# Performance work log

Measured on AMD Instinct MI355X. Metric: run time of the kernel, lower is better.

Reference implementation:

```python
import jax, jax.numpy as jnp
import numpy as np


def _dynamics(x, ts, W1, b1, tW, W2, b2, W3, b3):
    # 2-hidden-layer tanh MLP with additive time conditioning; works for [B,D] or [D].
    h = jnp.tanh(x @ W1 + b1 + ts * tW)
    h = jnp.tanh(h @ W2 + b2)
    return h @ W3 + b3


def setup_inputs() -> dict:
    key = jax.random.key(0)
    B, D, H = 1024, 256, 1024
    ks = jax.random.split(key, 8)
    scaled = lambda k, shape, fan: jax.random.normal(k, shape, jnp.float32) / np.float32(np.sqrt(fan))
    return {
        "x": jax.random.normal(ks[0], (B, D), jnp.float32),
        "t": jax.random.uniform(ks[1], (1,), jnp.float32),
        "ldj": jnp.zeros((B,), jnp.float32),
        "reg_term": jnp.zeros((B,), jnp.float32),
        "W1": scaled(ks[2], (D, H), D),
        "b1": jnp.zeros((H,), jnp.float32),
        "tW": scaled(ks[3], (H,), 1),
        "W2": scaled(ks[4], (H, H), H),
        "b2": jnp.zeros((H,), jnp.float32),
        "W3": scaled(ks[5], (H, D), H),
        "b3": jnp.zeros((D,), jnp.float32),
    }


def reference(x, t, ldj, reg_term, W1, b1, tW, W2, b2, W3, b3):
    ts = t[0]
    # dx = dynamics(x, t)
    dx = _dynamics(x, ts, W1, b1, tW, W2, b2, W3, b3)
    # exact trace of per-sample Jacobian d dynamics / dx  (trace_method='exact')
    f_single = lambda xi: _dynamics(xi, ts, W1, b1, tW, W2, b2, W3, b3)  # [D] -> [D]
    jac = jax.vmap(jax.jacfwd(f_single))(x)          # [B, D, D]
    ldj_out = jnp.trace(jac, axis1=1, axis2=2)       # [B]
    reg_out = jnp.zeros_like(ldj_out)                 # ode_regularization == 0
    return dx, ldj_out, reg_out
```

## Files before the change

kernel.cpp:

```cpp
#include <hip/hip_runtime.h>
#include <math.h>

#define Bsz 1024
#define Dsz 256
#define Hsz 1024

typedef unsigned short u16;
typedef __bf16 bf16x8 __attribute__((ext_vector_type(8)));
typedef float  f32x4  __attribute__((ext_vector_type(4)));

__device__ __forceinline__ float bf2f(u16 u) {
  unsigned v = ((unsigned)u) << 16;
  return __builtin_bit_cast(float, v);
}
__device__ __forceinline__ u16 f2bf(float f) {
  unsigned u = __builtin_bit_cast(unsigned, f);
  u += 0x7FFFu + ((u >> 16) & 1u);
  return (u16)(u >> 16);
}

__device__ __forceinline__ void cast_chunk(const float* __restrict__ in,
                                           u16* __restrict__ out, int b, int t) {
  const int i = b * 256 + t;
  const float4 v = reinterpret_cast<const float4*>(in)[i];
  ushort4 o;
  o.x = f2bf(v.x); o.y = f2bf(v.y); o.z = f2bf(v.z); o.w = f2bf(v.w);
  *reinterpret_cast<ushort4*>(&out[(size_t)i * 4]) = o;
}

__device__ __forceinline__ void tr_tile(float (*tl)[65], const float* __restrict__ in,
                                        u16* __restrict__ out, int R, int C,
                                        int c0, int r0, int t) {
#pragma unroll
  for (int p = 0; p < 4; ++p) {
    const int r = p * 16 + (t >> 4);
    const int c = (t & 15) * 4;
    const float4 v = *reinterpret_cast<const float4*>(&in[(size_t)(r0 + r) * C + c0 + c]);
    tl[r][c] = v.x; tl[r][c + 1] = v.y; tl[r][c + 2] = v.z; tl[r][c + 3] = v.w;
  }
  __syncthreads();
#pragma unroll
  for (int p = 0; p < 4; ++p) {
    const int a = p * 16 + (t >> 4);
    const int b4 = (t & 15) * 4;
    ushort4 o;
    o.x = f2bf(tl[b4 + 0][a]); o.y = f2bf(tl[b4 + 1][a]);
    o.z = f2bf(tl[b4 + 2][a]); o.w = f2bf(tl[b4 + 3][a]);
    *reinterpret_cast<ushort4*>(&out[(size_t)(c0 + a) * R + r0 + b4]) = o;
  }
}

__global__ __launch_bounds__(256) void prep(const float* __restrict__ x,
                                            const float* __restrict__ W1,
                                            const float* __restrict__ W2,
                                            const float* __restrict__ W3,
                                            u16* __restrict__ xb,
                                            u16* __restrict__ W3b,
                                            u16* __restrict__ W1bT,
                                            u16* __restrict__ W2bT,
                                            u16* __restrict__ W3bT,
                                            float* __restrict__ ldj) {
  __shared__ float tl[64][65];
  const int b = blockIdx.x, t = threadIdx.x;
  if (b == 0) {
    for (int i = t; i < 2048; i += 256) ldj[i] = 0.0f;
  }
  if (b < 256) {
    cast_chunk(x, xb, b, t);
  } else if (b < 512) {
    cast_chunk(W3, W3b, b - 256, t);
  } else if (b < 576) {
    const int tb = b - 512;
    tr_tile(tl, W1, W1bT, Dsz, Hsz, (tb & 15) * 64, (tb >> 4) * 64, t);
  } else if (b < 832) {
    const int tb = b - 576;
    tr_tile(tl, W2, W2bT, Hsz, Hsz, (tb & 15) * 64, (tb >> 4) * 64, t);
  } else {
    const int tb = b - 832;
    tr_tile(tl, W3, W3bT, Hsz, Dsz, (tb & 3) * 64, (tb >> 2) * 64, t);
  }
}

enum { EPI_H1 = 0, EPI_AMAT = 1, EPI_H2 = 2, EPI_DX = 3, EPI_TRACE = 4 };
constexpr int LS = 72;

template <int EPI, bool SQA>
__device__ __forceinline__ void gemm_body(
    int row0, int col0,
    u16* __restrict__ As, u16* __restrict__ Bs, float (*sred)[33],
    const u16* __restrict__ A, const u16* __restrict__ Bt,
    int K, int ldo,
    float* __restrict__ fout, u16* __restrict__ bout,
    const u16* __restrict__ aux,
    const float* __restrict__ v1, const float* __restrict__ v2,
    const float* __restrict__ tptr) {
  const int t = threadIdx.x;
  const int lane = t & 63, wid = t >> 6;

  const int sm = t >> 2, sq = t & 3;
  const size_t a_base = (size_t)(row0 + sm) * K + sq * 8;
  const size_t b_base = (size_t)(col0 + sm) * K + sq * 8;

  uint4 ar[2], br[2];
  auto load_regs = [&](int k0) {
    ar[0] = *reinterpret_cast<const uint4*>(&A[a_base + k0]);
    ar[1] = *reinterpret_cast<const uint4*>(&A[a_base + k0 + 32]);
    br[0] = *reinterpret_cast<const uint4*>(&Bt[b_base + k0]);
    br[1] = *reinterpret_cast<const uint4*>(&Bt[b_base + k0 + 32]);
  };
  auto sq_tr = [&](uint4 v) -> uint4 {
    u16* p = reinterpret_cast<u16*>(&v);
    uint4 o; u16* po = reinterpret_cast<u16*>(&o);
#pragma unroll
    for (int i = 0; i < 8; ++i) { const float h = bf2f(p[i]); po[i] = f2bf(1.0f - h * h); }
    return o;
  };
  auto store_lds = [&]() {
    const int ab = sm * LS + sq * 8;
#pragma unroll
    for (int c = 0; c < 2; ++c) {
      const uint4 av = SQA ? sq_tr(ar[c]) : ar[c];
      *reinterpret_cast<uint4*>(&As[ab + c * 32]) = av;
      *reinterpret_cast<uint4*>(&Bs[ab + c * 32]) = br[c];
    }
  };

  f32x4 acc[2][2] = {};
  const int mo = (wid >> 1) * 32, no = (wid & 1) * 32;
  const int fr = lane & 15, fg = lane >> 4;

  const int NK = K >> 6;
  load_regs(0);
  for (int it = 0; it < NK; ++it) {
    __syncthreads();
    store_lds();
    if (it + 1 < NK) load_regs((it + 1) << 6);
    __syncthreads();
#pragma unroll
    for (int ks = 0; ks < 64; ks += 32) {
      union { uint4 u; bf16x8 b; } cv;
      cv.u = *reinterpret_cast<const uint4*>(&As[(mo + fr) * LS + ks + fg * 8]);
      const bf16x8 a0 = cv.b;
      cv.u = *reinterpret_cast<const uint4*>(&As[(mo + 16 + fr) * LS + ks + fg * 8]);
      const bf16x8 a1 = cv.b;
      cv.u = *reinterpret_cast<const uint4*>(&Bs[(no + fr) * LS + ks + fg * 8]);
      const bf16x8 b0 = cv.b;
      cv.u = *reinterpret_cast<const uint4*>(&Bs[(no + 16 + fr) * LS + ks + fg * 8]);
      const bf16x8 b1 = cv.b;
      acc[0][0] = __builtin_amdgcn_mfma_f32_16x16x32_bf16(a0, b0, acc[0][0], 0, 0, 0);
      acc[0][1] = __builtin_amdgcn_mfma_f32_16x16x32_bf16(a0, b1, acc[0][1], 0, 0, 0);
      acc[1][0] = __builtin_amdgcn_mfma_f32_16x16x32_bf16(a1, b0, acc[1][0], 0, 0, 0);
      acc[1][1] = __builtin_amdgcn_mfma_f32_16x16x32_bf16(a1, b1, acc[1][1], 0, 0, 0);
    }
  }

  const int cr = mo + fg * 4;
  const int cc = no + fr;

  if (EPI == EPI_H1) {
    const float ts = tptr[0];
#pragma unroll
    for (int ni = 0; ni < 2; ++ni) {
      const int col = col0 + cc + ni * 16;
      const float add = v1[col] + ts * v2[col];
#pragma unroll
      for (int mi = 0; mi < 2; ++mi)
#pragma unroll
        for (int r = 0; r < 4; ++r) {
          const int row = row0 + cr + mi * 16 + r;
          bout[(size_t)row * Hsz + col] = f2bf(tanhf(acc[mi][ni][r] + add));
        }
    }
  } else if (EPI == EPI_AMAT) {
#pragma unroll
    for (int mi = 0; mi < 2; ++mi)
#pragma unroll
      for (int ni = 0; ni < 2; ++ni)
#pragma unroll
        for (int r = 0; r < 4; ++r) {
          const int row = row0 + cr + mi * 16 + r;
          const int col = col0 + cc + ni * 16;
          const float w2 = bf2f(aux[(size_t)row * Hsz + col]);
          bout[(size_t)row * Hsz + col] = f2bf(w2 * acc[mi][ni][r]);
        }
  } else if (EPI == EPI_H2) {
#pragma unroll
    for (int ni = 0; ni < 2; ++ni) {
      const int col = col0 + cc + ni * 16;
      const float add = v1[col];
#pragma unroll
      for (int mi = 0; mi < 2; ++mi)
#pragma unroll
        for (int r = 0; r < 4; ++r) {
          const int row = row0 + cr + mi * 16 + r;
          bout[(size_t)row * Hsz + col] = f2bf(tanhf(acc[mi][ni][r] + add));
        }
    }
  } else if (EPI == EPI_DX) {
#pragma unroll
    for (int ni = 0; ni < 2; ++ni) {
      const int col = col0 + cc + ni * 16;
      const float add = v1[col];
#pragma unroll
      for (int mi = 0; mi < 2; ++mi)
#pragma unroll
        for (int r = 0; r < 4; ++r) {
          const int row = row0 + cr + mi * 16 + r;
          fout[(size_t)row * ldo + col] = acc[mi][ni][r] + add;
        }
    }
  } else {
#pragma unroll
    for (int mi = 0; mi < 2; ++mi)
#pragma unroll
      for (int r = 0; r < 4; ++r) {
        const int row = row0 + cr + mi * 16 + r;
        float s = 0.f;
#pragma unroll
        for (int ni = 0; ni < 2; ++ni) {
          const int col = col0 + cc + ni * 16;
          const float h2 = bf2f(aux[(size_t)row * Hsz + col]);
          s += acc[mi][ni][r] * (1.0f - h2 * h2);
        }
        sred[cr + mi * 16 + r][(wid & 1) * 16 + fr] = s;
      }
    __syncthreads();
    if (t < 64) {
      float s = 0.f;
#pragma unroll
      for (int u = 0; u < 32; ++u) s += sred[t][u];
      atomicAdd(&fout[row0 + t], s);
    }
  }
}

__global__ __launch_bounds__(256) void phaseB(const u16* __restrict__ xb,
                                              const u16* __restrict__ W1bT,
                                              const u16* __restrict__ W3b,
                                              const u16* __restrict__ W2bT,
                                              u16* __restrict__ H1b,
                                              u16* __restrict__ AmatT,
                                              const float* __restrict__ b1,
                                              const float* __restrict__ tW,
                                              const float* __restrict__ t) {
  __shared__ u16 As[64 * LS];
  __shared__ u16 Bs[64 * LS];
  const int b = blockIdx.x;
  if (b < 256) {
    gemm_body<EPI_H1, false>((b >> 4) * 64, (b & 15) * 64, As, Bs, nullptr,
                             xb, W1bT, Dsz, Hsz, nullptr, H1b, nullptr, b1, tW, t);
  } else {
    const int c = b - 256;
    gemm_body<EPI_AMAT, false>((c >> 4) * 64, (c & 15) * 64, As, Bs, nullptr,
                               W3b, W1bT, Dsz, Hsz, nullptr, AmatT, W2bT,
                               nullptr, nullptr, nullptr);
  }
}

__global__ __launch_bounds__(256) void phaseC(const u16* __restrict__ H1b,
                                              const u16* __restrict__ W2bT,
                                              u16* __restrict__ H2b,
                                              const float* __restrict__ b2) {
  __shared__ u16 As[64 * LS];
  __shared__ u16 Bs[64 * LS];
  const int b = blockIdx.x;
  gemm_body<EPI_H2, false>((b >> 4) * 64, (b & 15) * 64, As, Bs, nullptr,
                           H1b, W2bT, Hsz, Hsz, nullptr, H2b, nullptr, b2,
                           nullptr, nullptr);
}

__global__ __launch_bounds__(256) void phaseD(const u16* __restrict__ H1b,
                                              const u16* __restrict__ AmatT,
                                              const u16* __restrict__ H2b,
                                              const u16* __restrict__ W3bT,
                                              float* __restrict__ ldj,
                                              float* __restrict__ dx,
                                              const float* __restrict__ b3) {
  __shared__ u16 As[64 * LS];
  __shared__ u16 Bs[64 * LS];
  __shared__ float sred[64][33];
  const int b = blockIdx.x;
  if (b < 256) {
    gemm_body<EPI_TRACE, true>((b >> 4) * 64, (b & 15) * 64, As, Bs, sred,
                               H1b, AmatT, Hsz, 0, ldj, nullptr, H2b,
                               nullptr, nullptr, nullptr);
  } else {
    const int c = b - 256;
    gemm_body<EPI_DX, false>((c >> 2) * 64, (c & 3) * 64, As, Bs, nullptr,
                             H2b, W3bT, Hsz, Dsz, dx, nullptr, nullptr, b3,
                             nullptr, nullptr);
  }
}

extern "C" void kernel_launch(void* const* d_in, const int* in_sizes, int n_in,
                              void* d_out, int out_size, void* d_ws, size_t ws_size,
                              hipStream_t stream) {
  const float* x  = (const float*)d_in[0];
  const float* t  = (const float*)d_in[1];
  const float* W1 = (const float*)d_in[4];
  const float* b1 = (const float*)d_in[5];
  const float* tW = (const float*)d_in[6];
  const float* W2 = (const float*)d_in[7];
  const float* b2 = (const float*)d_in[8];
  const float* W3 = (const float*)d_in[9];
  const float* b3 = (const float*)d_in[10];

  float* out = (float*)d_out;
  float* dx  = out;
  float* ldj = out + (size_t)Bsz * Dsz;

  u16* w = (u16*)d_ws;
  u16* xb    = w;
  u16* W1bT  = xb    + 262144;
  u16* W3b   = W1bT  + 262144;
  u16* W3bT  = W3b   + 262144;
  u16* W2bT  = W3bT  + 262144;
  u16* AmatT = W2bT  + 1048576;
  u16* H1b   = AmatT + 1048576;
  u16* H2b   = H1b   + 1048576;

  const dim3 blk(256);
  prep  <<<dim3(896), blk, 0, stream>>>(x, W1, W2, W3, xb, W3b, W1bT, W2bT, W3bT, ldj);
  phaseB<<<dim3(512), blk, 0, stream>>>(xb, W1bT, W3b, W2bT, H1b, AmatT, b1, tW, t);
  phaseC<<<dim3(256), blk, 0, stream>>>(H1b, W2bT, H2b, b2);
  phaseD<<<dim3(320), blk, 0, stream>>>(H1b, AmatT, H2b, W3bT, ldj, dx, b3);
}
```

Baseline: 133.9 us.

## Fuse paired GEMMs sharing operands and recompute H2 inside trace kernel

Merges the H1 and Amat GEMMs into one kernel that shares the W1 tile loads. It also merges the H2 GEMM with the trace GEMM: H1 tiles are loaded once, tanh is recomputed in registers, and H2 is written while the trace is accumulated without being re-read. The dx GEMM moves to a separate 64-block kernel, and block indices are swizzled for L2 locality. This cuts redundant global loads and one round trip for H2. In exchange there are fewer blocks per launch, more LDS per block, and a small dx launch that underfills the GPU.

```diff
diff --git a/kernel.cpp b/kernel.cpp
--- a/kernel.cpp
+++ b/kernel.cpp
@@ -18,6 +18,15 @@
   u += 0x7FFFu + ((u >> 16) & 1u);
   return (u16)(u >> 16);
 }
+
+constexpr int LS = 72;
+
+__device__ __forceinline__ bf16x8 frag(const u16* __restrict__ s, int row, int off) {
+  union { uint4 u; bf16x8 b; } cv;
+  cv.u = *reinterpret_cast<const uint4*>(&s[row * LS + off]);
+  return cv.b;
+}
+#define MFMA __builtin_amdgcn_mfma_f32_16x16x32_bf16
 
 __device__ __forceinline__ void cast_chunk(const float* __restrict__ in,
                                            u16* __restrict__ out, int b, int t) {
@@ -81,32 +90,119 @@
   }
 }
 
-enum { EPI_H1 = 0, EPI_AMAT = 1, EPI_H2 = 2, EPI_DX = 3, EPI_TRACE = 4 };
-constexpr int LS = 72;
-
-template <int EPI, bool SQA>
-__device__ __forceinline__ void gemm_body(
-    int row0, int col0,
-    u16* __restrict__ As, u16* __restrict__ Bs, float (*sred)[33],
-    const u16* __restrict__ A, const u16* __restrict__ Bt,
-    int K, int ldo,
-    float* __restrict__ fout, u16* __restrict__ bout,
-    const u16* __restrict__ aux,
-    const float* __restrict__ v1, const float* __restrict__ v2,
-    const float* __restrict__ tptr) {
+__global__ __launch_bounds__(256) void phaseBB(const u16* __restrict__ xb,
+                                               const u16* __restrict__ W3b,
+                                               const u16* __restrict__ W1bT,
+                                               const u16* __restrict__ W2bT,
+                                               u16* __restrict__ H1b,
+                                               u16* __restrict__ AmatT,
+                                               const float* __restrict__ b1,
+                                               const float* __restrict__ tW,
+                                               const float* __restrict__ tptr) {
+  __shared__ u16 A1s[64 * LS];
+  __shared__ u16 A2s[64 * LS];
+  __shared__ u16 Bs[64 * LS];
   const int t = threadIdx.x;
   const int lane = t & 63, wid = t >> 6;
+  const int bz = ((blockIdx.x & 7) << 5) + (blockIdx.x >> 3);
+  const int row0 = (bz >> 4) * 64, col0 = (bz & 15) * 64;
 
   const int sm = t >> 2, sq = t & 3;
-  const size_t a_base = (size_t)(row0 + sm) * K + sq * 8;
-  const size_t b_base = (size_t)(col0 + sm) * K + sq * 8;
-
-  uint4 ar[2], br[2];
+  const size_t ab = (size_t)(row0 + sm) * Dsz + sq * 8;
+  const size_t bb = (size_t)(col0 + sm) * Dsz + sq * 8;
+
+  uint4 a1r[2], a2r[2], br[2];
   auto load_regs = [&](int k0) {
-    ar[0] = *reinterpret_cast<const uint4*>(&A[a_base + k0]);
-    ar[1] = *reinterpret_cast<const uint4*>(&A[a_base + k0 + 32]);
-    br[0] = *reinterpret_cast<const uint4*>(&Bt[b_base + k0]);
-    br[1] = *reinterpret_cast<const uint4*>(&Bt[b_base + k0 + 32]);
+    a1r[0] = *reinterpret_cast<const uint4*>(&xb[ab + k0]);
+    a1r[1] = *reinterpret_cast<const uint4*>(&xb[ab + k0 + 32]);
+    a2r[0] = *reinterpret_cast<const uint4*>(&W3b[ab + k0]);
+    a2r[1] = *reinterpret_cast<const uint4*>(&W3b[ab + k0 + 32]);
+    br[0]  = *reinterpret_cast<const uint4*>(&W1bT[bb + k0]);
+    br[1]  = *reinterpret_cast<const uint4*>(&W1bT[bb + k0 + 32]);
+  };
+  auto store_lds = [&]() {
+    const int o = sm * LS + sq * 8;
+#pragma unroll
+    for (int c = 0; c < 2; ++c) {
+      *reinterpret_cast<uint4*>(&A1s[o + c * 32]) = a1r[c];
+      *reinterpret_cast<uint4*>(&A2s[o + c * 32]) = a2r[c];
+      *reinterpret_cast<uint4*>(&Bs[o + c * 32])  = br[c];
+    }
+  };
+
+  f32x4 acc1[2][2] = {}, acc2[2][2] = {};
+  const int mo = (wid >> 1) * 32, no = (wid & 1) * 32;
+  const int fr = lane & 15, fg = lane >> 4;
+
+  load_regs(0);
+  for (int it = 0; it < Dsz / 64; ++it) {
+    __syncthreads();
+    store_lds();
+    if (it + 1 < Dsz / 64) load_regs((it + 1) << 6);
+    __syncthreads();
+#pragma unroll
+    for (int ks = 0; ks < 64; ks += 32) {
+      const int off = ks + fg * 8;
+      const bf16x8 a10 = frag(A1s, mo + fr, off), a11 = frag(A1s, mo + 16 + fr, off);
+      const bf16x8 a20 = frag(A2s, mo + fr, off), a21 = frag(A2s, mo + 16 + fr, off);
+      const bf16x8 b0  = frag(Bs,  no + fr, off), b1v = frag(Bs,  no + 16 + fr, off);
+      acc1[0][0] = MFMA(a10, b0,  acc1[0][0], 0, 0, 0);
+      acc1[0][1] = MFMA(a10, b1v, acc1[0][1], 0, 0, 0);
+      acc1[1][0] = MFMA(a11, b0,  acc1[1][0], 0, 0, 0);
+      acc1[1][1] = MFMA(a11, b1v, acc1[1][1], 0, 0, 0);
+      acc2[0][0] = MFMA(a20, b0,  acc2[0][0], 0, 0, 0);
+      acc2[0][1] = MFMA(a20, b1v, acc2[0][1], 0, 0, 0);
+      acc2[1][0] = MFMA(a21, b0,  acc2[1][0], 0, 0, 0);
+      acc2[1][1] = MFMA(a21, b1v, acc2[1][1], 0, 0, 0);
+    }
+  }
+
+  const int cr = mo + fg * 4, cc = no + fr;
+  const float ts = tptr[0];
+#pragma unroll
+  for (int ni = 0; ni < 2; ++ni) {
+    const int col = col0 + cc + ni * 16;
+    const float add = b1[col] + ts * tW[col];
+#pragma unroll
+    for (int mi = 0; mi < 2; ++mi)
+#pragma unroll
+      for (int r = 0; r < 4; ++r) {
+        const int row = row0 + cr + mi * 16 + r;
+        H1b[(size_t)row * Hsz + col] = f2bf(tanhf(acc1[mi][ni][r] + add));
+        const float w2 = bf2f(W2bT[(size_t)row * Hsz + col]);
+        AmatT[(size_t)row * Hsz + col] = f2bf(w2 * acc2[mi][ni][r]);
+      }
+  }
+}
+
+__global__ __launch_bounds__(256) void phaseCD(const u16* __restrict__ H1b,
+                                               const u16* __restrict__ W2bT,
+                                               const u16* __restrict__ AmatT,
+                                               u16* __restrict__ H2b,
+                                               float* __restrict__ ldj,
+                                               const float* __restrict__ b2) {
+  __shared__ u16 Ars[64 * LS];
+  __shared__ u16 Ads[64 * LS];
+  __shared__ u16 B1s[64 * LS];
+  __shared__ u16 B2s[64 * LS];
+  __shared__ float sred[64][33];
+  const int t = threadIdx.x;
+  const int lane = t & 63, wid = t >> 6;
+  const int bz = ((blockIdx.x & 7) << 5) + (blockIdx.x >> 3);
+  const int row0 = (bz >> 4) * 64, col0 = (bz & 15) * 64;
+
+  const int sm = t >> 2, sq = t & 3;
+  const size_t ab = (size_t)(row0 + sm) * Hsz + sq * 8;
+  const size_t bb = (size_t)(col0 + sm) * Hsz + sq * 8;
+
+  uint4 ar[2], b1r[2], b2r[2];
+  auto load_regs = [&](int k0) {
+    ar[0]  = *reinterpret_cast<const uint4*>(&H1b[ab + k0]);
+    ar[1]  = *reinterpret_cast<const uint4*>(&H1b[ab + k0 + 32]);
+    b1r[0] = *reinterpret_cast<const uint4*>(&W2bT[bb + k0]);
+    b1r[1] = *reinterpret_cast<const uint4*>(&W2bT[bb + k0 + 32]);
+    b2r[0] = *reinterpret_cast<const uint4*>(&AmatT[bb + k0]);
+    b2r[1] = *reinterpret_cast<const uint4*>(&AmatT[bb + k0 + 32]);
   };
   auto sq_tr = [&](uint4 v) -> uint4 {
     u16* p = reinterpret_cast<u16*>(&v);
@@ -116,179 +212,134 @@
     return o;
   };
   auto store_lds = [&]() {
-    const int ab = sm * LS + sq * 8;
+    const int o = sm * LS + sq * 8;
 #pragma unroll
     for (int c = 0; c < 2; ++c) {
-      const uint4 av = SQA ? sq_tr(ar[c]) : ar[c];
-      *reinterpret_cast<uint4*>(&As[ab + c * 32]) = av;
-      *reinterpret_cast<uint4*>(&Bs[ab + c * 32]) = br[c];
-    }
-  };
-
-  f32x4 acc[2][2] = {};
+      *reinterpret_cast<uint4*>(&Ars[o + c * 32]) = ar[c];
+      *reinterpret_cast<uint4*>(&Ads[o + c * 32]) = sq_tr(ar[c]);
+      *reinterpret_cast<uint4*>(&B1s[o + c * 32]) = b1r[c];
+      *reinterpret_cast<uint4*>(&B2s[o + c * 32]) = b2r[c];
+    }
+  };
+
+  f32x4 acc1[2][2] = {}, acc2[2][2] = {};
   const int mo = (wid >> 1) * 32, no = (wid & 1) * 32;
   const int fr = lane & 15, fg = lane >> 4;
 
-  const int NK = K >> 6;
   load_regs(0);
-  for (int it = 0; it < NK; ++it) {
+  for (int it = 0; it < Hsz / 64; ++it) {
     __syncthreads();
     store_lds();
-    if (it + 1 < NK) load_regs((it + 1) << 6);
+    if (it + 1 < Hsz / 64) load_regs((it + 1) << 6);
     __syncthreads();
 #pragma unroll
     for (int ks = 0; ks < 64; ks += 32) {
-      union { uint4 u; bf16x8 b; } cv;
-      cv.u = *reinterpret_cast<const uint4*>(&As[(mo + fr) * LS + ks + fg * 8]);
-      const bf16x8 a0 = cv.b;
-      cv.u = *reinterpret_cast<const uint4*>(&As[(mo + 16 + fr) * LS + ks + fg * 8]);
-      const bf16x8 a1 = cv.b;
-      cv.u = *reinterpret_cast<const uint4*>(&Bs[(no + fr) * LS + ks + fg * 8]);
-      const bf16x8 b0 = cv.b;
-      cv.u = *reinterpret_cast<const uint4*>(&Bs[(no + 16 + fr) * LS + ks + fg * 8]);
-      const bf16x8 b1 = cv.b;
-      acc[0][0] = __builtin_amdgcn_mfma_f32_16x16x32_bf16(a0, b0, acc[0][0], 0, 0, 0);
-      acc[0][1] = __builtin_amdgcn_mfma_f32_16x16x32_bf16(a0, b1, acc[0][1], 0, 0, 0);
-      acc[1][0] = __builtin_amdgcn_mfma_f32_16x16x32_bf16(a1, b0, acc[1][0], 0, 0, 0);
-      acc[1][1] = __builtin_amdgcn_mfma_f32_16x16x32_bf16(a1, b1, acc[1][1], 0, 0, 0);
-    }
-  }
-
-  const int cr = mo + fg * 4;
-  const int cc = no + fr;
-
-  if (EPI == EPI_H1) {
-    const float ts = tptr[0];
-#pragma unroll
-    for (int ni = 0; ni < 2; ++ni) {
-      const int col = col0 + cc + ni * 16;
-      const float add = v1[col] + ts * v2[col];
-#pragma unroll
-      for (int mi = 0; mi < 2; ++mi)
-#pragma unroll
-        for (int r = 0; r < 4; ++r) {
-          const int row = row0 + cr + mi * 16 + r;
-          bout[(size_t)row * Hsz + col] = f2bf(tanhf(acc[mi][ni][r] + add));
-        }
-    }
-  } else if (EPI == EPI_AMAT) {
-#pragma unroll
-    for (int mi = 0; mi < 2; ++mi)
-#pragma unroll
-      for (int ni = 0; ni < 2; ++ni)
-#pragma unroll
-        for (int r = 0; r < 4; ++r) {
-          const int row = row0 + cr + mi * 16 + r;
-          const int col = col0 + cc + ni * 16;
-          const float w2 = bf2f(aux[(size_t)row * Hsz + col]);
-          bout[(size_t)row * Hsz + col] = f2bf(w2 * acc[mi][ni][r]);
-        }
-  } else if (EPI == EPI_H2) {
-#pragma unroll
-    for (int ni = 0; ni < 2; ++ni) {
-      const int col = col0 + cc + ni * 16;
-      const float add = v1[col];
-#pragma unroll
-      for (int mi = 0; mi < 2; ++mi)
-#pragma unroll
-        for (int r = 0; r < 4; ++r) {
-          const int row = row0 + cr + mi * 16 + r;
-          bout[(size_t)row * Hsz + col] = f2bf(tanhf(acc[mi][ni][r] + add));
-        }
-    }
-  } else if (EPI == EPI_DX) {
-#pragma unroll
-    for (int ni = 0; ni < 2; ++ni) {
-      const int col = col0 + cc + ni * 16;
-      const float add = v1[col];
-#pragma unroll
-      for (int mi = 0; mi < 2; ++mi)
-#pragma unroll
-        for (int r = 0; r < 4; ++r) {
-          const int row = row0 + cr + mi * 16 + r;
-          fout[(size_t)row * ldo + col] = acc[mi][ni][r] + add;
-        }
-    }
-  } else {
-#pragma unroll
-    for (int mi = 0; mi < 2; ++mi)
-#pragma unroll
-      for (int r = 0; r < 4; ++r) {
+      const int off = ks + fg * 8;
+      const bf16x8 x0 = frag(Ars, mo + fr, off), x1 = frag(Ars, mo + 16 + fr, off);
+      const bf16x8 d0 = frag(Ads, mo + fr, off), d1 = frag(Ads, mo + 16 + fr, off);
+      const bf16x8 w0 = frag(B1s, no + fr, off), w1 = frag(B1s, no + 16 + fr, off);
+      const bf16x8 m0 = frag(B2s, no + fr, off), m1 = frag(B2s, no + 16 + fr, off);
+      acc1[0][0] = MFMA(x0, w0, acc1[0][0], 0, 0, 0);
+      acc1[0][1] = MFMA(x0, w1, acc1[0][1], 0, 0, 0);
+      acc1[1][0] = MFMA(x1, w0, acc1[1][0], 0, 0, 0);
+      acc1[1][1] = MFMA(x1, w1, acc1[1][1], 0, 0, 0);
+      acc2[0][0] = MFMA(d0, m0, acc2[0][0], 0, 0, 0);
+      acc2[0][1] = MFMA(d0, m1, acc2[0][1], 0, 0, 0);
+      acc2[1][0] = MFMA(d1, m0, acc2[1][0], 0, 0, 0);
+      acc2[1][1] = MFMA(d1, m1, acc2[1][1], 0, 0, 0);
+    }
+  }
+
+  const int cr = mo + fg * 4, cc = no + fr;
+#pragma unroll
+  for (int mi = 0; mi < 2; ++mi)
+#pragma unroll
+    for (int r = 0; r < 4; ++r) {
+      float s = 0.f;
+#pragma unroll
+      for (int ni = 0; ni < 2; ++ni) {
+        const int col = col0 + cc + ni * 16;
         const int row = row0 + cr + mi * 16 + r;
-        float s = 0.f;
-#pragma unroll
-        for (int ni = 0; ni < 2; ++ni) {
-          const int col = col0 + cc + ni * 16;
-          const float h2 = bf2f(aux[(size_t)row * Hsz + col]);
-          s += acc[mi][ni][r] * (1.0f - h2 * h2);
-        }
-        sred[cr + mi * 16 + r][(wid & 1) * 16 + fr] = s;
+        const float h = tanhf(acc1[mi][ni][r] + b2[col]);
+        H2b[(size_t)row * Hsz + col] = f2bf(h);
+        s += acc2[mi][ni][r] * (1.0f - h * h);
       }
-    __syncthreads();
-    if (t < 64) {
-      float s = 0.f;
-#pragma unroll
-      for (int u = 0; u < 32; ++u) s += sred[t][u];
-      atomicAdd(&fout[row0 + t], s);
-    }
-  }
-}
-
-__global__ __launch_bounds__(256) void phaseB(const u16* __restrict__ xb,
-                                              const u16* __restrict__ W1bT,
-                                              const u16* __restrict__ W3b,
-                                              const u16* __restrict__ W2bT,
-                                              u16* __restrict__ H1b,
-                                              u16* __restrict__ AmatT,
-                                              const float* __restrict__ b1,
-                                              const float* __restrict__ tW,
-                                              const float* __restrict__ t) {
-  __shared__ u16 As[64 * LS];
-  __shared__ u16 Bs[64 * LS];
-  const int b = blockIdx.x;
-  if (b < 256) {
-    gemm_body<EPI_H1, false>((b >> 4) * 64, (b & 15) * 64, As, Bs, nullptr,
-                             xb, W1bT, Dsz, Hsz, nullptr, H1b, nullptr, b1, tW, t);
-  } else {
-    const int c = b - 256;
-    gemm_body<EPI_AMAT, false>((c >> 4) * 64, (c & 15) * 64, As, Bs, nullptr,
-                               W3b, W1bT, Dsz, Hsz, nullptr, AmatT, W2bT,
-                               nullptr, nullptr, nullptr);
-  }
-}
-
-__global__ __launch_bounds__(256) void phaseC(const u16* __restrict__ H1b,
-                                              const u16* __restrict__ W2bT,
-                                              u16* __restrict__ H2b,
-                                              const float* __restrict__ b2) {
-  __shared__ u16 As[64 * LS];
-  __shared__ u16 Bs[64 * LS];
-  const int b = blockIdx.x;
-  gemm_body<EPI_H2, false>((b >> 4) * 64, (b & 15) * 64, As, Bs, nullptr,
-                           H1b, W2bT, Hsz, Hsz, nullptr, H2b, nullptr, b2,
-                           nullptr, nullptr);
-}
-
-__global__ __launch_bounds__(256) void phaseD(const u16* __restrict__ H1b,
-                                              const u16* __restrict__ AmatT,
-                                              const u16* __restrict__ H2b,
+      sred[cr + mi * 16 + r][(wid & 1) * 16 + fr] = s;
+    }
+  __syncthreads();
+  if (t < 64) {
+    float s = 0.f;
+#pragma unroll
+    for (int u = 0; u < 32; ++u) s += sred[t][u];
+    atomicAdd(&ldj[row0 + t], s);
+  }
+}
+
+__global__ __launch_bounds__(256) void phaseE(const u16* __restrict__ H2b,
                                               const u16* __restrict__ W3bT,
-                                              float* __restrict__ ldj,
                                               float* __restrict__ dx,
                                               const float* __restrict__ b3) {
   __shared__ u16 As[64 * LS];
   __shared__ u16 Bs[64 * LS];
-  __shared__ float sred[64][33];
-  const int b = blockIdx.x;
-  if (b < 256) {
-    gemm_body<EPI_TRACE, true>((b >> 4) * 64, (b & 15) * 64, As, Bs, sred,
-                               H1b, AmatT, Hsz, 0, ldj, nullptr, H2b,
-                               nullptr, nullptr, nullptr);
-  } else {
-    const int c = b - 256;
-    gemm_body<EPI_DX, false>((c >> 2) * 64, (c & 3) * 64, As, Bs, nullptr,
-                             H2b, W3bT, Hsz, Dsz, dx, nullptr, nullptr, b3,
-                             nullptr, nullptr);
+  const int t = threadIdx.x;
+  const int lane = t & 63, wid = t >> 6;
+  const int bz = ((blockIdx.x & 7) << 3) + (blockIdx.x >> 3);
+  const int row0 = (bz >> 2) * 64, col0 = (bz & 3) * 64;
+
+  const int sm = t >> 2, sq = t & 3;
+  const size_t ab = (size_t)(row0 + sm) * Hsz + sq * 8;
+  const size_t bb = (size_t)(col0 + sm) * Hsz + sq * 8;
+
+  uint4 ar[2], br[2];
+  auto load_regs = [&](int k0) {
+    ar[0] = *reinterpret_cast<const uint4*>(&H2b[ab + k0]);
+    ar[1] = *reinterpret_cast<const uint4*>(&H2b[ab + k0 + 32]);
+    br[0] = *reinterpret_cast<const uint4*>(&W3bT[bb + k0]);
+    br[1] = *reinterpret_cast<const uint4*>(&W3bT[bb + k0 + 32]);
+  };
+  auto store_lds = [&]() {
+    const int o = sm * LS + sq * 8;
+#pragma unroll
+    for (int c = 0; c < 2; ++c) {
+      *reinterpret_cast<uint4*>(&As[o + c * 32]) = ar[c];
+      *reinterpret_cast<uint4*>(&Bs[o + c * 32]) = br[c];
+    }
+  };
+
+  f32x4 acc[2][2] = {};
+  const int mo = (wid >> 1) * 32, no = (wid & 1) * 32;
+  const int fr = lane & 15, fg = lane >> 4;
+
+  load_regs(0);
+  for (int it = 0; it < Hsz / 64; ++it) {
+    __syncthreads();
+    store_lds();
+    if (it + 1 < Hsz / 64) load_regs((it + 1) << 6);
+    __syncthreads();
+#pragma unroll
+    for (int ks = 0; ks < 64; ks += 32) {
+      const int off = ks + fg * 8;
+      const bf16x8 a0 = frag(As, mo + fr, off), a1 = frag(As, mo + 16 + fr, off);
+      const bf16x8 b0 = frag(Bs, no + fr, off), b1v = frag(Bs, no + 16 + fr, off);
+      acc[0][0] = MFMA(a0, b0,  acc[0][0], 0, 0, 0);
+      acc[0][1] = MFMA(a0, b1v, acc[0][1], 0, 0, 0);
+      acc[1][0] = MFMA(a1, b0,  acc[1][0], 0, 0, 0);
+      acc[1][1] = MFMA(a1, b1v, acc[1][1], 0, 0, 0);
+    }
+  }
+
+  const int cr = mo + fg * 4, cc = no + fr;
+#pragma unroll
+  for (int ni = 0; ni < 2; ++ni) {
+    const int col = col0 + cc + ni * 16;
+    const float add = b3[col];
+#pragma unroll
+    for (int mi = 0; mi < 2; ++mi)
+#pragma unroll
+      for (int r = 0; r < 4; ++r) {
+        const int row = row0 + cr + mi * 16 + r;
+        dx[(size_t)row * Dsz + col] = acc[mi][ni][r] + add;
+      }
   }
 }
 
@@ -320,8 +371,8 @@
   u16* H2b   = H1b   + 1048576;
 
   const dim3 blk(256);
-  prep  <<<dim3(896), blk, 0, stream>>>(x, W1, W2, W3, xb, W3b, W1bT, W2bT, W3bT, ldj);
-  phaseB<<<dim3(512), blk, 0, stream>>>(xb, W1bT, W3b, W2bT, H1b, AmatT, b1, tW, t);
-  phaseC<<<dim3(256), blk, 0, stream>>>(H1b, W2bT, H2b, b2);
-  phaseD<<<dim3(320), blk, 0, stream>>>(H1b, AmatT, H2b, W3bT, ldj, dx, b3);
-}
+  prep   <<<dim3(896), blk, 0, stream>>>(x, W1, W2, W3, xb, W3b, W1bT, W2bT, W3bT, ldj);
+  phaseBB<<<dim3(256), blk, 0, stream>>>(xb, W3b, W1bT, W2bT, H1b, AmatT, b1, tW, t);
+  phaseCD<<<dim3(256), blk, 0, stream>>>(H1b, W2bT, AmatT, H2b, ldj, b2);
+  phaseE <<<dim3(64),  blk, 0, stream>>>(H2b, W3bT, dx, b3);
+}
```

Result: slower. 159.5 us (+19.1%).

## Move trace GEMM into phase C and reduce trace in a light phase D

Applied to the files above, without the earlier changes.

The large trace GEMM (H1' times AmatT) moves from phaseD into phaseC, where it runs alongside the H2 GEMM because it does not depend on H2. It writes an fp32 intermediate U, and a small reduction in phaseD multiplies U by (1-h2^2) and sums each row into ldj. This removes the serial tail where phaseD ran 256 heavy GEMM blocks after phaseC, and drops the per-block atomics. In exchange it adds a 4 MB fp32 write and read of U. Note the SQA path still applies 1-h^2 to H1, and ldj is now written directly rather than accumulated.

```diff
diff --git a/kernel.cpp b/kernel.cpp
--- a/kernel.cpp
+++ b/kernel.cpp
@@ -18,6 +18,15 @@
   u += 0x7FFFu + ((u >> 16) & 1u);
   return (u16)(u >> 16);
 }
+
+constexpr int LS = 72;
+
+__device__ __forceinline__ bf16x8 frag(const u16* __restrict__ s, int row, int off) {
+  union { uint4 u; bf16x8 b; } cv;
+  cv.u = *reinterpret_cast<const uint4*>(&s[row * LS + off]);
+  return cv.b;
+}
+#define MFMA __builtin_amdgcn_mfma_f32_16x16x32_bf16
 
 __device__ __forceinline__ void cast_chunk(const float* __restrict__ in,
                                            u16* __restrict__ out, int b, int t) {
@@ -81,13 +90,12 @@
   }
 }
 
-enum { EPI_H1 = 0, EPI_AMAT = 1, EPI_H2 = 2, EPI_DX = 3, EPI_TRACE = 4 };
-constexpr int LS = 72;
+enum { EPI_H1 = 0, EPI_AMAT = 1, EPI_H2 = 2, EPI_DX = 3, EPI_U = 4 };
 
 template <int EPI, bool SQA>
 __device__ __forceinline__ void gemm_body(
     int row0, int col0,
-    u16* __restrict__ As, u16* __restrict__ Bs, float (*sred)[33],
+    u16* __restrict__ As, u16* __restrict__ Bs,
     const u16* __restrict__ A, const u16* __restrict__ Bt,
     int K, int ldo,
     float* __restrict__ fout, u16* __restrict__ bout,
@@ -116,12 +124,11 @@
     return o;
   };
   auto store_lds = [&]() {
-    const int ab = sm * LS + sq * 8;
+    const int o = sm * LS + sq * 8;
 #pragma unroll
     for (int c = 0; c < 2; ++c) {
-      const uint4 av = SQA ? sq_tr(ar[c]) : ar[c];
-      *reinterpret_cast<uint4*>(&As[ab + c * 32]) = av;
-      *reinterpret_cast<uint4*>(&Bs[ab + c * 32]) = br[c];
+      *reinterpret_cast<uint4*>(&As[o + c * 32]) = SQA ? sq_tr(ar[c]) : ar[c];
+      *reinterpret_cast<uint4*>(&Bs[o + c * 32]) = br[c];
     }
   };
 
@@ -138,19 +145,13 @@
     __syncthreads();
 #pragma unroll
     for (int ks = 0; ks < 64; ks += 32) {
-      union { uint4 u; bf16x8 b; } cv;
-      cv.u = *reinterpret_cast<const uint4*>(&As[(mo + fr) * LS + ks + fg * 8]);
-      const bf16x8 a0 = cv.b;
-      cv.u = *reinterpret_cast<const uint4*>(&As[(mo + 16 + fr) * LS + ks + fg * 8]);
-      const bf16x8 a1 = cv.b;
-      cv.u = *reinterpret_cast<const uint4*>(&Bs[(no + fr) * LS + ks + fg * 8]);
-      const bf16x8 b0 = cv.b;
-      cv.u = *reinterpret_cast<const uint4*>(&Bs[(no + 16 + fr) * LS + ks + fg * 8]);
-      const bf16x8 b1 = cv.b;
-      acc[0][0] = __builtin_amdgcn_mfma_f32_16x16x32_bf16(a0, b0, acc[0][0], 0, 0, 0);
-      acc[0][1] = __builtin_amdgcn_mfma_f32_16x16x32_bf16(a0, b1, acc[0][1], 0, 0, 0);
-      acc[1][0] = __builtin_amdgcn_mfma_f32_16x16x32_bf16(a1, b0, acc[1][0], 0, 0, 0);
-      acc[1][1] = __builtin_amdgcn_mfma_f32_16x16x32_bf16(a1, b1, acc[1][1], 0, 0, 0);
+      const int off = ks + fg * 8;
+      const bf16x8 a0 = frag(As, mo + fr, off), a1 = frag(As, mo + 16 + fr, off);
+      const bf16x8 b0 = frag(Bs, no + fr, off), b1v = frag(Bs, no + 16 + fr, off);
+      acc[0][0] = MFMA(a0, b0,  acc[0][0], 0, 0, 0);
+      acc[0][1] = MFMA(a0, b1v, acc[0][1], 0, 0, 0);
+      acc[1][0] = MFMA(a1, b0,  acc[1][0], 0, 0, 0);
+      acc[1][1] = MFMA(a1, b1v, acc[1][1], 0, 0, 0);
     }
   }
 
@@ -211,25 +212,15 @@
     }
   } else {
 #pragma unroll
-    for (int mi = 0; mi < 2; ++mi)
-#pragma unroll
-      for (int r = 0; r < 4; ++r) {
-        const int row = row0 + cr + mi * 16 + r;
-        float s = 0.f;
-#pragma unroll
-        for (int ni = 0; ni < 2; ++ni) {
-          const int col = col0 + cc + ni * 16;
-          const float h2 = bf2f(aux[(size_t)row * Hsz + col]);
-          s += acc[mi][ni][r] * (1.0f - h2 * h2);
-        }
-        sred[cr + mi * 16 + r][(wid & 1) * 16 + fr] = s;
-      }
-    __syncthreads();
-    if (t < 64) {
-      float s = 0.f;
-#pragma unroll
-      for (int u = 0; u < 32; ++u) s += sred[t][u];
-      atomicAdd(&fout[row0 + t], s);
+    for (int ni = 0; ni < 2; ++ni) {
+      const int col = col0 + cc + ni * 16;
+#pragma unroll
+      for (int mi = 0; mi < 2; ++mi)
+#pragma unroll
+        for (int r = 0; r < 4; ++r) {
+          const int row = row0 + cr + mi * 16 + r;
+          fout[(size_t)row * Hsz + col] = acc[mi][ni][r];
+        }
     }
   }
 }
@@ -247,48 +238,73 @@
   __shared__ u16 Bs[64 * LS];
   const int b = blockIdx.x;
   if (b < 256) {
-    gemm_body<EPI_H1, false>((b >> 4) * 64, (b & 15) * 64, As, Bs, nullptr,
+    gemm_body<EPI_H1, false>((b >> 4) * 64, (b & 15) * 64, As, Bs,
                              xb, W1bT, Dsz, Hsz, nullptr, H1b, nullptr, b1, tW, t);
   } else {
     const int c = b - 256;
-    gemm_body<EPI_AMAT, false>((c >> 4) * 64, (c & 15) * 64, As, Bs, nullptr,
+    gemm_body<EPI_AMAT, false>((c >> 4) * 64, (c & 15) * 64, As, Bs,
                                W3b, W1bT, Dsz, Hsz, nullptr, AmatT, W2bT,
                                nullptr, nullptr, nullptr);
   }
 }
 
-__global__ __launch_bounds__(256) void phaseC(const u16* __restrict__ H1b,
-                                              const u16* __restrict__ W2bT,
-                                              u16* __restrict__ H2b,
-                                              const float* __restrict__ b2) {
+__global__ __launch_bounds__(256) void phaseCU(const u16* __restrict__ H1b,
+                                               const u16* __restrict__ W2bT,
+                                               const u16* __restrict__ AmatT,
+                                               u16* __restrict__ H2b,
+                                               float* __restrict__ U,
+                                               const float* __restrict__ b2) {
   __shared__ u16 As[64 * LS];
   __shared__ u16 Bs[64 * LS];
   const int b = blockIdx.x;
-  gemm_body<EPI_H2, false>((b >> 4) * 64, (b & 15) * 64, As, Bs, nullptr,
-                           H1b, W2bT, Hsz, Hsz, nullptr, H2b, nullptr, b2,
-                           nullptr, nullptr);
-}
-
-__global__ __launch_bounds__(256) void phaseD(const u16* __restrict__ H1b,
-                                              const u16* __restrict__ AmatT,
-                                              const u16* __restrict__ H2b,
+  if (b < 256) {
+    gemm_body<EPI_H2, false>((b >> 4) * 64, (b & 15) * 64, As, Bs,
+                             H1b, W2bT, Hsz, Hsz, nullptr, H2b, nullptr, b2,
+                             nullptr, nullptr);
+  } else {
+    const int c = b - 256;
+    gemm_body<EPI_U, true>((c >> 4) * 64, (c & 15) * 64, As, Bs,
+                           H1b, AmatT, Hsz, Hsz, U, nullptr, nullptr,
+                           nullptr, nullptr, nullptr);
+  }
+}
+
+__global__ __launch_bounds__(256) void phaseD(const u16* __restrict__ H2b,
                                               const u16* __restrict__ W3bT,
+                                              const float* __restrict__ U,
+                                              float* __restrict__ dx,
                                               float* __restrict__ ldj,
-                                              float* __restrict__ dx,
                                               const float* __restrict__ b3) {
-  __shared__ u16 As[64 * LS];
-  __shared__ u16 Bs[64 * LS];
-  __shared__ float sred[64][33];
   const int b = blockIdx.x;
-  if (b < 256) {
-    gemm_body<EPI_TRACE, true>((b >> 4) * 64, (b & 15) * 64, As, Bs, sred,
-                               H1b, AmatT, Hsz, 0, ldj, nullptr, H2b,
-                               nullptr, nullptr, nullptr);
-  } else {
-    const int c = b - 256;
-    gemm_body<EPI_DX, false>((c >> 2) * 64, (c & 3) * 64, As, Bs, nullptr,
+  if (b < 64) {
+    __shared__ u16 As[64 * LS];
+    __shared__ u16 Bs[64 * LS];
+    gemm_body<EPI_DX, false>((b >> 2) * 64, (b & 3) * 64, As, Bs,
                              H2b, W3bT, Hsz, Dsz, dx, nullptr, nullptr, b3,
                              nullptr, nullptr);
+  } else {
+    __shared__ float sr[16][17];
+    const int t = threadIdx.x;
+    const int row = (b - 64) * 16 + (t >> 4);
+    const int c0 = (t & 15) * 4;
+    float s = 0.0f;
+#pragma unroll
+    for (int k = 0; k < 16; ++k) {
+      const int c = c0 + k * 64;
+      const float4 u4 = *reinterpret_cast<const float4*>(&U[(size_t)row * Hsz + c]);
+      const ushort4 h4 = *reinterpret_cast<const ushort4*>(&H2b[(size_t)row * Hsz + c]);
+      const float h0 = bf2f(h4.x), h1 = bf2f(h4.y), h2 = bf2f(h4.z), h3 = bf2f(h4.w);
+      s += u4.x * (1.0f - h0 * h0) + u4.y * (1.0f - h1 * h1)
+         + u4.z * (1.0f - h2 * h2) + u4.w * (1.0f - h3 * h3);
+    }
+    sr[t >> 4][t & 15] = s;
+    __syncthreads();
+    if (t < 16) {
+      float tot = 0.0f;
+#pragma unroll
+      for (int u = 0; u < 16; ++u) tot += sr[t][u];
+      ldj[(b - 64) * 16 + t] = tot;
+    }
   }
 }
 
@@ -318,10 +334,11 @@
   u16* AmatT = W2bT  + 1048576;
   u16* H1b   = AmatT + 1048576;
   u16* H2b   = H1b   + 1048576;
+  float* U   = (float*)(H2b + 1048576);
 
   const dim3 blk(256);
-  prep  <<<dim3(896), blk, 0, stream>>>(x, W1, W2, W3, xb, W3b, W1bT, W2bT, W3bT, ldj);
-  phaseB<<<dim3(512), blk, 0, stream>>>(xb, W1bT, W3b, W2bT, H1b, AmatT, b1, tW, t);
-  phaseC<<<dim3(256), blk, 0, stream>>>(H1b, W2bT, H2b, b2);
-  phaseD<<<dim3(320), blk, 0, stream>>>(H1b, AmatT, H2b, W3bT, ldj, dx, b3);
-}
+  prep   <<<dim3(896), blk, 0, stream>>>(x, W1, W2, W3, xb, W3b, W1bT, W2bT, W3bT, ldj);
+  phaseB <<<dim3(512), blk, 0, stream>>>(xb, W1bT, W3b, W2bT, H1b, AmatT, b1, tW, t);
+  phaseCU<<<dim3(512), blk, 0, stream>>>(H1b, W2bT, AmatT, H2b, U, b2);
+  phaseD <<<dim3(128), blk, 0, stream>>>(H2b, W3bT, U, dx, ldj, b3);
+}
```

Measured after the change: 131.8 us. About the same (-1.6%).
